# Optimization experiments

Measured on AMD Instinct MI355X. Metric: run time of the kernel, lower is better.

Reference implementation:

```python
import jax, jax.numpy as jnp
import numpy as np

B, S, D, H, HD, FFN_MULT = 4, 2048, 2048, 16, 128, 4
EPS = 1e-8


def setup_inputs() -> dict:
    key = jax.random.key(0)
    ks = jax.random.split(key, 12)
    s = lambda k, shape, scale: (jax.random.normal(k, shape, dtype=jnp.float32) * scale)
    d_ff = D * FFN_MULT
    return {
        "x": s(ks[0], (B, S, D), 1.0),
        # per-head Q/K/V projections, stacked: [H, D, HD] (no bias, as in source)
        "wq": s(ks[1], (H, D, HD), D ** -0.5),
        "wk": s(ks[2], (H, D, HD), D ** -0.5),
        "wv": s(ks[3], (H, D, HD), D ** -0.5),
        # output projection Linear(D, D) with bias
        "wo": s(ks[4], (D, D), D ** -0.5),
        "bo": jnp.zeros((D,), jnp.float32),
        # FFN: Linear(D, d_ff) -> ReLU -> Linear(d_ff, D), both with bias
        "w1": s(ks[5], (D, d_ff), D ** -0.5),
        "b1": jnp.zeros((d_ff,), jnp.float32),
        "w2": s(ks[6], (d_ff, D), d_ff ** -0.5),
        "b2": jnp.zeros((D,), jnp.float32),
        # RMSNorm gains
        "g1": jnp.ones((D,), jnp.float32),
        "g2": jnp.ones((D,), jnp.float32),
    }


def rms_norm(x, g):
    return x * jax.lax.rsqrt(jnp.mean(x * x, axis=-1, keepdims=True) + EPS) * g


def attention(h, wq, wk, wv, wo, bo):
    # per-head projections batched over heads: [B,S,D] x [H,D,K] -> [B,H,S,K]
    q = jnp.einsum("bsd,hdk->bhsk", h, wq)
    k = jnp.einsum("bsd,hdk->bhsk", h, wk)
    v = jnp.einsum("bsd,hdk->bhsk", h, wv)
    scores = jnp.einsum("bhsk,bhtk->bhst", q, k) * (HD ** -0.5)
    causal = jnp.tril(jnp.ones((S, S), dtype=bool))
    scores = jnp.where(causal, scores, -jnp.inf)
    attn = jax.nn.softmax(scores, axis=-1)
    out = jnp.einsum("bhst,bhtk->bhsk", attn, v)  # [B,H,S,HD]
    # concat heads along feature dim (head order matches torch.cat over heads)
    out = out.transpose(0, 2, 1, 3).reshape(B, S, D)
    return out @ wo + bo


def reference(x, wq, wk, wv, wo, bo, w1, b1, w2, b2, g1, g2):
    x = x + attention(rms_norm(x, g1), wq, wk, wv, wo, bo)
    h = rms_norm(x, g2)
    ffn = jax.nn.relu(h @ w1 + b1) @ w2 + b2
    return x + ffn
```

## Files before the change

kernel.cpp:

```cpp
#include <hip/hip_runtime.h>
#include <hip/hip_bf16.h>

#define Bsz 4
#define Ssz 2048
#define Dsz 2048
#define Hn 16
#define HDsz 128
#define DFF 8192
#define Msz (Bsz*Ssz)

typedef __bf16 bf16x8 __attribute__((ext_vector_type(8)));
typedef float  f32x4  __attribute__((ext_vector_type(4)));

enum { FLAG_BIAS=1, FLAG_RELU=2, FLAG_RESID=4, FLAG_F32OUT=8 };

#define GLDS16(g, l) __builtin_amdgcn_global_load_lds( \
    (const __attribute__((address_space(1))) unsigned int*)(g), \
    (__attribute__((address_space(3))) unsigned int*)(l), 16, 0, 0)

template <typename TIN>
__global__ __launch_bounds__(256) void transpose_cvt(
    const TIN* __restrict__ in, __bf16* __restrict__ out,
    int R, int C, long long inRS, int subB,
    long long strideOuter, long long strideInner, long long outBS)
{
  __shared__ float tile[32][33];
  int bz = blockIdx.z;
  const TIN* inp = in + (size_t)(bz / subB) * strideOuter + (size_t)(bz % subB) * strideInner;
  __bf16* outp = out + (size_t)bz * outBS;
  int tx = threadIdx.x, ty = threadIdx.y;
  int c  = blockIdx.x * 32 + tx;
  int r0 = blockIdx.y * 32;
#pragma unroll
  for (int i = 0; i < 4; ++i) {
    int r = r0 + ty + i * 8;
    tile[ty + i * 8][tx] = (float)inp[(size_t)r * inRS + c];
  }
  __syncthreads();
  int oc  = r0 + tx;
  int or0 = blockIdx.x * 32;
#pragma unroll
  for (int i = 0; i < 4; ++i) {
    int orr = or0 + ty + i * 8;
    outp[(size_t)orr * R + oc] = (__bf16)tile[tx][ty + i * 8];
  }
}

__global__ __launch_bounds__(256) void rmsnorm_k(
    const float* __restrict__ x, const float* __restrict__ g, __bf16* __restrict__ out)
{
  int row = blockIdx.x, tid = threadIdx.x;
  const float4* xr = (const float4*)(x + (size_t)row * Dsz);
  float4 v0 = xr[tid*2], v1 = xr[tid*2+1];
  float ss = v0.x*v0.x + v0.y*v0.y + v0.z*v0.z + v0.w*v0.w
           + v1.x*v1.x + v1.y*v1.y + v1.z*v1.z + v1.w*v1.w;
#pragma unroll
  for (int off = 32; off > 0; off >>= 1) ss += __shfl_down(ss, off);
  __shared__ float wsum[4];
  __shared__ float sc;
  if ((tid & 63) == 0) wsum[tid >> 6] = ss;
  __syncthreads();
  if (tid == 0) {
    float t = wsum[0] + wsum[1] + wsum[2] + wsum[3];
    sc = rsqrtf(t * (1.0f / (float)Dsz) + 1e-8f);
  }
  __syncthreads();
  float s = sc;
  const float4* gr = (const float4*)g;
  float4 g0 = gr[tid*2], g1v = gr[tid*2+1];
  bf16x8 ov;
  ov[0]=(__bf16)(v0.x*s*g0.x);  ov[1]=(__bf16)(v0.y*s*g0.y);
  ov[2]=(__bf16)(v0.z*s*g0.z);  ov[3]=(__bf16)(v0.w*s*g0.w);
  ov[4]=(__bf16)(v1.x*s*g1v.x); ov[5]=(__bf16)(v1.y*s*g1v.y);
  ov[6]=(__bf16)(v1.z*s*g1v.z); ov[7]=(__bf16)(v1.w*s*g1v.w);
  *(bf16x8*)(out + (size_t)row * Dsz + tid * 8) = ov;
}

#define SBAR       asm volatile("s_barrier" ::: "memory")
#define WAIT_VM2   asm volatile("s_waitcnt vmcnt(2)" ::: "memory")
#define WAIT_VM0   asm volatile("s_waitcnt vmcnt(0)" ::: "memory")

#define STG1(Xb, Xlds, buf, kst) \
    GLDS16((Xb) + (size_t)rloc * K + (kst) + sloc, (Xlds) + (buf)*16384 + wuni)

#define LDA(mi) (*(const bf16x8*)(AsB + cur*16384 + (wr*64 + (mi)*16 + l15)*64 + psl))
#define LDB(nj) (*(const bf16x8*)(BsB + cur*16384 + (wc*64 + (nj)*16 + l15)*64 + psl))

__global__ __launch_bounds__(1024) void gemm256(
    const __bf16* __restrict__ A, const __bf16* __restrict__ B,
    const float* __restrict__ bias, const float* __restrict__ resid,
    void* __restrict__ Cout, int M, int N, int K, int flags)
{
  __shared__ __align__(16) __bf16 As[3*256*32];
  __shared__ __align__(16) __bf16 Bs[3*256*32];
  int nwg = gridDim.x;
  int id = blockIdx.x;
  id = (id & 7) * (nwg >> 3) + (id >> 3);
  int ntn = N >> 8;
  int tm = id / ntn, tn = id - tm * ntn;
  int tid = threadIdx.x;
  int lane = tid & 63, w = tid >> 6;
  int l15 = lane & 15, lg = lane >> 4;
  int wr = w >> 2, wc = w & 3;
  const __bf16* Ab = A + (size_t)tm * 256 * K;
  const __bf16* Bb = B + (size_t)tn * 256 * K;
  char* AsB = (char*)As;
  char* BsB = (char*)Bs;
  int rloc = tid >> 2;
  int sloc = ((lane & 3) ^ ((lane >> 3) & 3)) * 8;
  int wuni = w * 1024;
  int psl  = (lg ^ ((l15 >> 1) & 3)) * 16;
  f32x4 zero; zero[0]=0.f; zero[1]=0.f; zero[2]=0.f; zero[3]=0.f;
  f32x4 acc[4][4];
#pragma unroll
  for (int i = 0; i < 4; ++i)
#pragma unroll
    for (int j = 0; j < 4; ++j) acc[i][j] = zero;
  int NT = K >> 5;
  STG1(Ab, AsB, 0, 0);
  STG1(Bb, BsB, 0, 0);
  STG1(Ab, AsB, 1, 32);
  STG1(Bb, BsB, 1, 32);
  WAIT_VM2; SBAR;
  int cur = 0;
  for (int t = 0; t < NT; ++t) {
    int sb = cur + 2; if (sb >= 3) sb -= 3;
    int kst = (t + 2 < NT) ? ((t + 2) << 5) : 0;
    STG1(Ab, AsB, sb, kst);
    STG1(Bb, BsB, sb, kst);
    bf16x8 af[4], bf[4];
    af[0]=LDA(0); af[1]=LDA(1); af[2]=LDA(2); af[3]=LDA(3);
    bf[0]=LDB(0); bf[1]=LDB(1); bf[2]=LDB(2); bf[3]=LDB(3);
#pragma unroll
    for (int mi = 0; mi < 4; ++mi)
#pragma unroll
      for (int nj = 0; nj < 4; ++nj)
        acc[mi][nj] = __builtin_amdgcn_mfma_f32_16x16x32_bf16(af[mi], bf[nj], acc[mi][nj], 0, 0, 0);
    WAIT_VM2;
    SBAR;
    cur += 1; if (cur >= 3) cur -= 3;
  }
  WAIT_VM0;
  int cm = tm * 256 + wr * 64;
  int cn = tn * 256 + wc * 64;
  float*  Cf = (float*)Cout;
  __bf16* Cb = (__bf16*)Cout;
#pragma unroll
  for (int m = 0; m < 4; ++m) {
#pragma unroll
    for (int nj = 0; nj < 4; ++nj) {
      int col = cn + nj * 16 + l15;
      float bv = (flags & FLAG_BIAS) ? bias[col] : 0.0f;
#pragma unroll
      for (int r = 0; r < 4; ++r) {
        int row = cm + m * 16 + 4 * lg + r;
        float v = acc[m][nj][r] + bv;
        if (flags & FLAG_RELU) v = v > 0.f ? v : 0.f;
        size_t idx = (size_t)row * N + col;
        if (flags & FLAG_RESID) v += resid[idx];
        if (flags & FLAG_F32OUT) Cf[idx] = v;
        else                     Cb[idx] = (__bf16)v;
      }
    }
  }
}

__global__ __launch_bounds__(512) void fattn(
    const __bf16* __restrict__ q, const __bf16* __restrict__ k,
    const __bf16* __restrict__ vt, __bf16* __restrict__ o)
{
  __shared__ __align__(16) __bf16 Ks[64*128];
  __shared__ __align__(16) __bf16 Vs[128*64];
  __shared__ __align__(16) __bf16 Ps[8][16*80];
  int bx = blockIdx.x, bh = blockIdx.y;
  int b = bh >> 4, h = bh & 15;
  int tid = threadIdx.x, lane = tid & 63, w = tid >> 6;
  int l15 = lane & 15, lg = lane >> 4;
  size_t base = ((size_t)b * Ssz) * Dsz + (size_t)h * HDsz;
  size_t vtb  = (size_t)bh * HDsz * Ssz;
  const float scale = 0.08838834764831845f;
  char* KsB = (char*)Ks;
  char* VsB = (char*)Vs;
  f32x4 zero; zero[0]=0.f; zero[1]=0.f; zero[2]=0.f; zero[3]=0.f;

  for (int ph = 0; ph < 2; ++ph) {
    int qt = ph ? bx : (15 - bx);
    int qs = qt * 128;
    int qmin = qs + w * 16;
    bf16x8 qf[4];
    int qrow = qmin + l15;
#pragma unroll
    for (int kk = 0; kk < 4; ++kk)
      qf[kk] = *(const bf16x8*)(q + base + (size_t)qrow * Dsz + kk * 32 + lg * 8);
    f32x4 acc[8];
#pragma unroll
    for (int i = 0; i < 8; ++i) acc[i] = zero;
    float mr[4], lr[4];
#pragma unroll
    for (int r = 0; r < 4; ++r) { mr[r] = -1e30f; lr[r] = 0.f; }
    int NT = 2 * qt + 2;
    for (int kt = 0; kt < NT; ++kt) {
      int t0 = kt * 64;
#pragma unroll
      for (int j = 0; j < 2; ++j) {
        int c = tid + j * 512;
        int tr = c >> 4, hc = c & 15;
        bf16x8 tk = *(const bf16x8*)(k + base + (size_t)(t0 + tr) * Dsz + hc * 8);
        *(bf16x8*)(KsB + ((tr * 256 + hc * 16) ^ ((tr & 7) << 4))) = tk;
        int hd = c >> 3, tc = c & 7;
        bf16x8 tv = *(const bf16x8*)(vt + vtb + (size_t)hd * Ssz + t0 + tc * 8);
        *(bf16x8*)(VsB + ((hd * 128 + tc * 16) ^ ((hd & 7) << 4))) = tv;
      }
      __syncthreads();
      bool act = (t0 <= qmin + 15);
      if (act) {
        f32x4 s[4];
#pragma unroll
        for (int cg = 0; cg < 4; ++cg) s[cg] = zero;
#pragma unroll
        for (int kk = 0; kk < 4; ++kk) {
#pragma unroll
          for (int cg = 0; cg < 4; ++cg) {
            int tl = cg * 16 + l15;
            bf16x8 kf = *(const bf16x8*)(KsB + ((tl * 256 + kk * 64 + lg * 16) ^ ((tl & 7) << 4)));
            s[cg] = __builtin_amdgcn_mfma_f32_16x16x32_bf16(qf[kk], kf, s[cg], 0, 0, 0);
          }
        }
        bool nm = (t0 + 63 > qmin);
        float pv[4][4];
        float al[4];
#pragma unroll
        for (int r = 0; r < 4; ++r) {
          int qr = qmin + 4 * lg + r;
          float rm = -1e30f;
#pragma unroll
          for (int cg = 0; cg < 4; ++cg) {
            float sv = s[cg][r] * scale;
            if (nm && (t0 + cg * 16 + l15) > qr) sv = -1e30f;
            s[cg][r] = sv;
            rm = fmaxf(rm, sv);
          }
          rm = fmaxf(rm, __shfl_xor(rm, 1));
          rm = fmaxf(rm, __shfl_xor(rm, 2));
          rm = fmaxf(rm, __shfl_xor(rm, 4));
          rm = fmaxf(rm, __shfl_xor(rm, 8));
          float mn = fmaxf(mr[r], rm);
          float a = __expf(mr[r] - mn);
          mr[r] = mn;
          float ps = 0.f;
#pragma unroll
          for (int cg = 0; cg < 4; ++cg) {
            float p = __expf(s[cg][r] - mn);
            pv[cg][r] = p;
            ps += p;
          }
          ps += __shfl_xor(ps, 1);
          ps += __shfl_xor(ps, 2);
          ps += __shfl_xor(ps, 4);
          ps += __shfl_xor(ps, 8);
          lr[r] = lr[r] * a + ps;
          al[r] = a;
        }
        f32x4 av; av[0]=al[0]; av[1]=al[1]; av[2]=al[2]; av[3]=al[3];
#pragma unroll
        for (int hg = 0; hg < 8; ++hg) acc[hg] *= av;
#pragma unroll
        for (int cg = 0; cg < 4; ++cg)
#pragma unroll
          for (int r = 0; r < 4; ++r)
            Ps[w][(4 * lg + r) * 80 + cg * 16 + l15] = (__bf16)pv[cg][r];
#pragma unroll
        for (int tt = 0; tt < 2; ++tt) {
          bf16x8 pf = *(const bf16x8*)(&Ps[w][l15 * 80 + tt * 32 + lg * 8]);
#pragma unroll
          for (int hg = 0; hg < 8; ++hg) {
            int hd = hg * 16 + l15;
            bf16x8 vf = *(const bf16x8*)(VsB + ((hd * 128 + tt * 64 + lg * 16) ^ ((hd & 7) << 4)));
            acc[hg] = __builtin_amdgcn_mfma_f32_16x16x32_bf16(pf, vf, acc[hg], 0, 0, 0);
          }
        }
      }
      __syncthreads();
    }
    f32x4 inv;
#pragma unroll
    for (int r = 0; r < 4; ++r) inv[r] = 1.0f / lr[r];
#pragma unroll
    for (int hg = 0; hg < 8; ++hg) {
      f32x4 ov = acc[hg] * inv;
#pragma unroll
      for (int r = 0; r < 4; ++r) {
        int qr2 = qmin + 4 * lg + r;
        o[base + (size_t)qr2 * Dsz + hg * 16 + l15] = (__bf16)ov[r];
      }
    }
  }
}

extern "C" void kernel_launch(void* const* d_in, const int* in_sizes, int n_in,
                              void* d_out, int out_size, void* d_ws, size_t ws_size,
                              hipStream_t stream)
{
  (void)in_sizes; (void)n_in; (void)out_size; (void)ws_size;
  const float* x  = (const float*)d_in[0];
  const float* wq = (const float*)d_in[1];
  const float* wk = (const float*)d_in[2];
  const float* wv = (const float*)d_in[3];
  const float* wo = (const float*)d_in[4];
  const float* bo = (const float*)d_in[5];
  const float* w1 = (const float*)d_in[6];
  const float* b1 = (const float*)d_in[7];
  const float* w2 = (const float*)d_in[8];
  const float* b2 = (const float*)d_in[9];
  const float* g1 = (const float*)d_in[10];
  const float* g2 = (const float*)d_in[11];
  float* out = (float*)d_out;
  char* ws = (char*)d_ws;

  const size_t U = (size_t)2048 * 2048 * 2;
  __bf16* wqT = (__bf16*)(ws);
  __bf16* wkT = (__bf16*)(ws + U);
  __bf16* wvT = (__bf16*)(ws + 2*U);
  __bf16* woT = (__bf16*)(ws + 3*U);
  __bf16* w1T = (__bf16*)(ws + 4*U);
  __bf16* w2T = (__bf16*)(ws + 8*U);
  __bf16* h1  = (__bf16*)(ws + 12*U);
  __bf16* vb  = (__bf16*)(ws + 16*U);
  __bf16* vT    = h1;
  __bf16* attno = vb;
  __bf16* fb    = h1;
  __bf16* h2    = (__bf16*)(ws);
  __bf16* qb = (__bf16*)d_out;
  __bf16* kb = qb + (size_t)Msz * Dsz;
  float*  x2 = (float*)d_out;

  dim3 tb(32, 8, 1);
  transpose_cvt<float><<<dim3(4,64,16),  tb, 0, stream>>>(wq, wqT, 2048, 128, 128, 1, (long long)2048*128, 0, (long long)128*2048);
  transpose_cvt<float><<<dim3(4,64,16),  tb, 0, stream>>>(wk, wkT, 2048, 128, 128, 1, (long long)2048*128, 0, (long long)128*2048);
  transpose_cvt<float><<<dim3(4,64,16),  tb, 0, stream>>>(wv, wvT, 2048, 128, 128, 1, (long long)2048*128, 0, (long long)128*2048);
  transpose_cvt<float><<<dim3(64,64,1),  tb, 0, stream>>>(wo, woT, 2048, 2048, 2048, 1, 0, 0, 0);
  transpose_cvt<float><<<dim3(256,64,1), tb, 0, stream>>>(w1, w1T, 2048, 8192, 8192, 1, 0, 0, 0);
  transpose_cvt<float><<<dim3(64,128,2), tb, 0, stream>>>(w2, w2T, 4096, 2048, 2048, 1, (long long)4096*2048, 0, (long long)2048*4096);
  rmsnorm_k<<<8192, 256, 0, stream>>>(x, g1, h1);
  gemm256<<<256, 1024, 0, stream>>>(h1, wqT, nullptr, nullptr, qb, Msz, 2048, 2048, 0);
  gemm256<<<256, 1024, 0, stream>>>(h1, wkT, nullptr, nullptr, kb, Msz, 2048, 2048, 0);
  gemm256<<<256, 1024, 0, stream>>>(h1, wvT, nullptr, nullptr, vb, Msz, 2048, 2048, 0);
  transpose_cvt<__bf16><<<dim3(4,64,64), tb, 0, stream>>>(vb, vT, 2048, 128, 2048, 16, (long long)2048*2048, 128, (long long)128*2048);
  fattn<<<dim3(8, 64), 512, 0, stream>>>(qb, kb, vT, attno);
  gemm256<<<256, 1024, 0, stream>>>(attno, woT, bo, x, x2, Msz, 2048, 2048, FLAG_BIAS | FLAG_RESID | FLAG_F32OUT);
  rmsnorm_k<<<8192, 256, 0, stream>>>(x2, g2, h2);
  for (int c = 0; c < 2; ++c) {
    gemm256<<<512, 1024, 0, stream>>>(h2, w1T + (size_t)c*4096*2048, b1 + c*4096, nullptr,
                                      fb, Msz, 4096, 2048, FLAG_BIAS | FLAG_RELU);
    int fl = FLAG_RESID | FLAG_F32OUT | (c == 0 ? FLAG_BIAS : 0);
    gemm256<<<256, 1024, 0, stream>>>(fb, w2T + (size_t)c*2048*4096, b2, x2,
                                      out, Msz, 2048, 4096, fl);
  }
}
```

Baseline: 1.346 ms.

## Fuse QKV GEMMs into one launch and add lazy rescaling in flash attention

The three separate Q/K/V projection GEMMs become one N=6144 GEMM whose epilogue routes each column block to the q, k or v buffer. This assumes wqT, wkT and wvT sit next to each other in the workspace. The attention kernel now rescales the accumulator only when the running max grows by more than a threshold, writes P straight to LDS with a narrower row stride, and raises wave priority around the MFMA sections. Together these aim to cut launch overhead and tail effects, plus softmax VALU and exp work, at the cost of a looser, lazily updated running-max invariant.

```diff
diff --git a/kernel.cpp b/kernel.cpp
--- a/kernel.cpp
+++ b/kernel.cpp
@@ -12,7 +12,7 @@
 typedef __bf16 bf16x8 __attribute__((ext_vector_type(8)));
 typedef float  f32x4  __attribute__((ext_vector_type(4)));
 
-enum { FLAG_BIAS=1, FLAG_RELU=2, FLAG_RESID=4, FLAG_F32OUT=8 };
+enum { FLAG_BIAS=1, FLAG_RELU=2, FLAG_RESID=4, FLAG_F32OUT=8, FLAG_QKV=16 };
 
 #define GLDS16(g, l) __builtin_amdgcn_global_load_lds( \
     (const __attribute__((address_space(1))) unsigned int*)(g), \
@@ -89,7 +89,8 @@
 __global__ __launch_bounds__(1024) void gemm256(
     const __bf16* __restrict__ A, const __bf16* __restrict__ B,
     const float* __restrict__ bias, const float* __restrict__ resid,
-    void* __restrict__ Cout, int M, int N, int K, int flags)
+    void* __restrict__ Cout, void* __restrict__ CoutV,
+    int M, int N, int K, int flags)
 {
   __shared__ __align__(16) __bf16 As[3*256*32];
   __shared__ __align__(16) __bf16 Bs[3*256*32];
@@ -144,19 +145,29 @@
   int cm = tm * 256 + wr * 64;
   int cn = tn * 256 + wc * 64;
   float*  Cf = (float*)Cout;
-  __bf16* Cb = (__bf16*)Cout;
+  __bf16* Cb;
+  int Ns = N, cnb = cn;
+  if (flags & FLAG_QKV) {
+    int which = cn >> 11;
+    Cb = (which == 2) ? (__bf16*)CoutV
+                      : ((__bf16*)Cout + (size_t)which * Msz * 2048);
+    Ns = 2048; cnb = cn & 2047;
+  } else {
+    Cb = (__bf16*)Cout;
+  }
 #pragma unroll
   for (int m = 0; m < 4; ++m) {
 #pragma unroll
     for (int nj = 0; nj < 4; ++nj) {
-      int col = cn + nj * 16 + l15;
+      int col  = cn  + nj * 16 + l15;
+      int colo = cnb + nj * 16 + l15;
       float bv = (flags & FLAG_BIAS) ? bias[col] : 0.0f;
 #pragma unroll
       for (int r = 0; r < 4; ++r) {
         int row = cm + m * 16 + 4 * lg + r;
         float v = acc[m][nj][r] + bv;
         if (flags & FLAG_RELU) v = v > 0.f ? v : 0.f;
-        size_t idx = (size_t)row * N + col;
+        size_t idx = (size_t)row * Ns + colo;
         if (flags & FLAG_RESID) v += resid[idx];
         if (flags & FLAG_F32OUT) Cf[idx] = v;
         else                     Cb[idx] = (__bf16)v;
@@ -171,7 +182,7 @@
 {
   __shared__ __align__(16) __bf16 Ks[64*128];
   __shared__ __align__(16) __bf16 Vs[128*64];
-  __shared__ __align__(16) __bf16 Ps[8][16*80];
+  __shared__ __align__(16) __bf16 Ps[8][16*72];
   int bx = blockIdx.x, bh = blockIdx.y;
   int b = bh >> 4, h = bh & 15;
   int tid = threadIdx.x, lane = tid & 63, w = tid >> 6;
@@ -217,6 +228,7 @@
         f32x4 s[4];
 #pragma unroll
         for (int cg = 0; cg < 4; ++cg) s[cg] = zero;
+        __builtin_amdgcn_s_setprio(1);
 #pragma unroll
         for (int kk = 0; kk < 4; ++kk) {
 #pragma unroll
@@ -226,52 +238,60 @@
             s[cg] = __builtin_amdgcn_mfma_f32_16x16x32_bf16(qf[kk], kf, s[cg], 0, 0, 0);
           }
         }
+        __builtin_amdgcn_s_setprio(0);
         bool nm = (t0 + 63 > qmin);
-        float pv[4][4];
-        float al[4];
+        float rm[4];
+        bool sk = true;
 #pragma unroll
         for (int r = 0; r < 4; ++r) {
           int qr = qmin + 4 * lg + r;
-          float rm = -1e30f;
+          float m0 = -1e30f;
 #pragma unroll
           for (int cg = 0; cg < 4; ++cg) {
             float sv = s[cg][r] * scale;
             if (nm && (t0 + cg * 16 + l15) > qr) sv = -1e30f;
             s[cg][r] = sv;
-            rm = fmaxf(rm, sv);
-          }
-          rm = fmaxf(rm, __shfl_xor(rm, 1));
-          rm = fmaxf(rm, __shfl_xor(rm, 2));
-          rm = fmaxf(rm, __shfl_xor(rm, 4));
-          rm = fmaxf(rm, __shfl_xor(rm, 8));
-          float mn = fmaxf(mr[r], rm);
-          float a = __expf(mr[r] - mn);
-          mr[r] = mn;
+            m0 = fmaxf(m0, sv);
+          }
+          m0 = fmaxf(m0, __shfl_xor(m0, 1));
+          m0 = fmaxf(m0, __shfl_xor(m0, 2));
+          m0 = fmaxf(m0, __shfl_xor(m0, 4));
+          m0 = fmaxf(m0, __shfl_xor(m0, 8));
+          rm[r] = m0;
+          sk = sk && (m0 <= mr[r] + 8.0f);
+        }
+        if (!__all(sk)) {
+          f32x4 av;
+#pragma unroll
+          for (int r = 0; r < 4; ++r) {
+            float mn = fmaxf(mr[r], rm[r]);
+            float a = __expf(mr[r] - mn);
+            mr[r] = mn;
+            lr[r] *= a;
+            av[r] = a;
+          }
+#pragma unroll
+          for (int hg = 0; hg < 8; ++hg) acc[hg] *= av;
+        }
+#pragma unroll
+        for (int r = 0; r < 4; ++r) {
           float ps = 0.f;
 #pragma unroll
           for (int cg = 0; cg < 4; ++cg) {
-            float p = __expf(s[cg][r] - mn);
-            pv[cg][r] = p;
+            float p = __expf(s[cg][r] - mr[r]);
+            Ps[w][(4 * lg + r) * 72 + cg * 16 + l15] = (__bf16)p;
             ps += p;
           }
           ps += __shfl_xor(ps, 1);
           ps += __shfl_xor(ps, 2);
           ps += __shfl_xor(ps, 4);
           ps += __shfl_xor(ps, 8);
-          lr[r] = lr[r] * a + ps;
-          al[r] = a;
-        }
-        f32x4 av; av[0]=al[0]; av[1]=al[1]; av[2]=al[2]; av[3]=al[3];
-#pragma unroll
-        for (int hg = 0; hg < 8; ++hg) acc[hg] *= av;
-#pragma unroll
-        for (int cg = 0; cg < 4; ++cg)
-#pragma unroll
-          for (int r = 0; r < 4; ++r)
-            Ps[w][(4 * lg + r) * 80 + cg * 16 + l15] = (__bf16)pv[cg][r];
+          lr[r] += ps;
+        }
+        __builtin_amdgcn_s_setprio(1);
 #pragma unroll
         for (int tt = 0; tt < 2; ++tt) {
-          bf16x8 pf = *(const bf16x8*)(&Ps[w][l15 * 80 + tt * 32 + lg * 8]);
+          bf16x8 pf = *(const bf16x8*)((char*)&Ps[w][0] + l15 * 144 + tt * 64 + lg * 16);
 #pragma unroll
           for (int hg = 0; hg < 8; ++hg) {
             int hd = hg * 16 + l15;
@@ -279,6 +299,7 @@
             acc[hg] = __builtin_amdgcn_mfma_f32_16x16x32_bf16(pf, vf, acc[hg], 0, 0, 0);
           }
         }
+        __builtin_amdgcn_s_setprio(0);
       }
       __syncthreads();
     }
@@ -342,18 +363,16 @@
   transpose_cvt<float><<<dim3(256,64,1), tb, 0, stream>>>(w1, w1T, 2048, 8192, 8192, 1, 0, 0, 0);
   transpose_cvt<float><<<dim3(64,128,2), tb, 0, stream>>>(w2, w2T, 4096, 2048, 2048, 1, (long long)4096*2048, 0, (long long)2048*4096);
   rmsnorm_k<<<8192, 256, 0, stream>>>(x, g1, h1);
-  gemm256<<<256, 1024, 0, stream>>>(h1, wqT, nullptr, nullptr, qb, Msz, 2048, 2048, 0);
-  gemm256<<<256, 1024, 0, stream>>>(h1, wkT, nullptr, nullptr, kb, Msz, 2048, 2048, 0);
-  gemm256<<<256, 1024, 0, stream>>>(h1, wvT, nullptr, nullptr, vb, Msz, 2048, 2048, 0);
+  gemm256<<<768, 1024, 0, stream>>>(h1, wqT, nullptr, nullptr, qb, vb, Msz, 6144, 2048, FLAG_QKV);
   transpose_cvt<__bf16><<<dim3(4,64,64), tb, 0, stream>>>(vb, vT, 2048, 128, 2048, 16, (long long)2048*2048, 128, (long long)128*2048);
   fattn<<<dim3(8, 64), 512, 0, stream>>>(qb, kb, vT, attno);
-  gemm256<<<256, 1024, 0, stream>>>(attno, woT, bo, x, x2, Msz, 2048, 2048, FLAG_BIAS | FLAG_RESID | FLAG_F32OUT);
+  gemm256<<<256, 1024, 0, stream>>>(attno, woT, bo, x, x2, nullptr, Msz, 2048, 2048, FLAG_BIAS | FLAG_RESID | FLAG_F32OUT);
   rmsnorm_k<<<8192, 256, 0, stream>>>(x2, g2, h2);
   for (int c = 0; c < 2; ++c) {
     gemm256<<<512, 1024, 0, stream>>>(h2, w1T + (size_t)c*4096*2048, b1 + c*4096, nullptr,
-                                      fb, Msz, 4096, 2048, FLAG_BIAS | FLAG_RELU);
+                                      fb, nullptr, Msz, 4096, 2048, FLAG_BIAS | FLAG_RELU);
     int fl = FLAG_RESID | FLAG_F32OUT | (c == 0 ? FLAG_BIAS : 0);
     gemm256<<<256, 1024, 0, stream>>>(fb, w2T + (size_t)c*2048*4096, b2, x2,
-                                      out, Msz, 2048, 4096, fl);
-  }
-}
+                                      out, nullptr, Msz, 2048, 4096, fl);
+  }
+}
```

Result: faster. 1.318 ms (-2.1%).
